# Kernel optimization log

Measured on AMD Instinct MI355X. Metric: run time of the kernel, lower is better.

Reference implementation:

```python
import jax, jax.numpy as jnp
import numpy as np

# Cayley-Dickson octonion multiplication tables (from the source module)
SIGN_TABLE = np.array([
    [+1, -1, -1, -1, -1, -1, -1, -1],
    [+1, +1, +1, -1, +1, -1, -1, +1],
    [+1, -1, +1, +1, +1, +1, -1, -1],
    [+1, +1, -1, +1, +1, -1, +1, -1],
    [+1, -1, -1, -1, +1, +1, +1, +1],
    [+1, +1, -1, +1, -1, +1, -1, +1],
    [+1, +1, +1, -1, -1, +1, +1, -1],
    [+1, -1, +1, +1, -1, -1, +1, +1],
], dtype=np.float32)
WEIGHT_IDX = np.array([
    [0, 1, 2, 3, 4, 5, 6, 7],
    [1, 0, 3, 2, 5, 4, 7, 6],
    [2, 3, 0, 1, 6, 7, 4, 5],
    [3, 2, 1, 0, 7, 6, 5, 4],
    [4, 5, 6, 7, 0, 1, 2, 3],
    [5, 4, 7, 6, 1, 0, 3, 2],
    [6, 7, 4, 5, 2, 3, 0, 1],
    [7, 6, 5, 4, 3, 2, 1, 0],
], dtype=np.int32)

B, T, D_IN, D_OUT = 4, 2048, 4096, 4096
K = D_IN // 8   # per-component input dim
N = D_OUT // 8  # per-component output dim


def setup_inputs() -> dict:
    key = jax.random.key(0)
    k1, k2 = jax.random.split(key)
    x = jax.random.normal(k1, (B, T, D_IN), dtype=jnp.float32)
    weight = jax.random.normal(k2, (8, N, K), dtype=jnp.float32) * (1.0 / np.sqrt(K))
    return {"x": x, "weight": weight}


def reference(x, weight):
    """Fused octonion (Cayley-Dickson) linear layer.

    y_i = sum_j sign[i,j] * x_j @ W[widx[i,j]].T
    x components are contiguous chunks of the last dim: x_j = x[..., j*K:(j+1)*K].
    """
    b, t, f = x.shape
    k = f // 8
    xs = x.reshape(b, t, 8, k)                 # [B,T,8,K], component axis j
    Wg = weight[jnp.asarray(WEIGHT_IDX)]        # [8(i),8(j),N,K] gathered weights
    S = jnp.asarray(SIGN_TABLE, dtype=x.dtype)  # [8(i),8(j)]
    # contract over j (component) and k (features); produce [B,T,i,N]
    y = jnp.einsum('ij,btjk,ijnk->btin', S, xs, Wg)
    return y.reshape(b, t, -1)                  # [B,T,8*N]
```

## Files before the change

### kernel.cpp

```cpp
#include <hip/hip_runtime.h>
#include <stdint.h>

typedef __attribute__((ext_vector_type(8))) short bf16x8;
typedef __attribute__((ext_vector_type(4))) float f32x4;

#define D_IN  4096
#define D_OUT 4096
#define KC 512
#define NC 512
#define NT 64

__constant__ float c_sign[64] = {
 +1,-1,-1,-1,-1,-1,-1,-1,
 +1,+1,+1,-1,+1,-1,-1,+1,
 +1,-1,+1,+1,+1,+1,-1,-1,
 +1,+1,-1,+1,+1,-1,+1,-1,
 +1,-1,-1,-1,+1,+1,+1,+1,
 +1,+1,-1,+1,-1,+1,-1,+1,
 +1,+1,+1,-1,-1,+1,+1,-1,
 +1,-1,+1,+1,-1,-1,+1,+1,
};

__device__ inline unsigned int pack2bf16(float a, float b) {
    unsigned int ua = __builtin_bit_cast(unsigned int, a);
    unsigned int ub = __builtin_bit_cast(unsigned int, b);
    ua = (ua + 0x7FFFu + ((ua >> 16) & 1u)) >> 16;
    ub = (ub + 0x7FFFu + ((ub >> 16) & 1u)) >> 16;
    return ua | (ub << 16);
}

typedef __attribute__((address_space(1))) const unsigned int gas_u32;
typedef __attribute__((address_space(3))) unsigned int las_u32;
#define ASYNC16(g, l) __builtin_amdgcn_global_load_lds((gas_u32*)(g), (las_u32*)(l), 16, 0, 0)
#define ENDP do { __builtin_amdgcn_s_barrier(); asm volatile("" ::: "memory"); } while (0)


__global__ __launch_bounds__(256)
void conv_x(const float* __restrict__ in, unsigned short* __restrict__ out, int n8) {
    int i = blockIdx.x * blockDim.x + threadIdx.x;
    if (i >= n8) return;
    const float4 a = ((const float4*)in)[(size_t)i * 2];
    const float4 b = ((const float4*)in)[(size_t)i * 2 + 1];
    uint4 o;
    o.x = pack2bf16(a.x, a.y); o.y = pack2bf16(a.z, a.w);
    o.z = pack2bf16(b.x, b.y); o.w = pack2bf16(b.z, b.w);
    ((uint4*)out)[i] = o;
}

__global__ __launch_bounds__(256)
void conv_w(const float* __restrict__ W, unsigned short* __restrict__ out) {
    int gid = blockIdx.x * blockDim.x + threadIdx.x;
    int row = gid >> 9;
    int c8  = gid & 511;
    int i = row >> 9, n = row & 511;
    int j = c8 >> 6;
    int k = (c8 & 63) << 3;
    float sgn = c_sign[i * 8 + j];
    const float* src = W + ((((i ^ j) * NC + n) * KC) + k);
    float4 a = *(const float4*)(src);
    float4 b = *(const float4*)(src + 4);
    uint4 o;
    o.x = pack2bf16(a.x * sgn, a.y * sgn); o.y = pack2bf16(a.z * sgn, a.w * sgn);
    o.z = pack2bf16(b.x * sgn, b.y * sgn); o.w = pack2bf16(b.z * sgn, b.w * sgn);
    ((uint4*)out)[gid] = o;
}


__device__ __forceinline__ void read_a(bf16x8 (&d)[4], const unsigned short* buf,
                                       int mh, int kk, int lane, int wr) {
#pragma unroll
    for (int f = 0; f < 4; ++f) {
        const int r  = wr * 128 + (mh * 4 + f) * 16 + (lane & 15);
        const int ch = (kk * 4 + (lane >> 4)) ^ (r & 7);
        d[f] = *(const bf16x8*)((const char*)buf + r * 128 + (ch << 4));
    }
}

__device__ __forceinline__ void read_b(bf16x8 (&d)[4], const unsigned short* buf,
                                       int kk, int lane, int wc) {
#pragma unroll
    for (int n = 0; n < 4; ++n) {
        const int r  = wc * 64 + n * 16 + (lane & 15);
        const int ch = (kk * 4 + (lane >> 4)) ^ (r & 7);
        d[n] = *(const bf16x8*)((const char*)buf + r * 128 + (ch << 4));
    }
}

__device__ __forceinline__ void mfma16(f32x4 (&acc)[8][4], int mh,
                                       const bf16x8 (&a)[4], const bf16x8 (&b)[4]) {
#pragma unroll
    for (int f = 0; f < 4; ++f)
#pragma unroll
        for (int n = 0; n < 4; ++n)
            acc[mh * 4 + f][n] = __builtin_amdgcn_mfma_f32_16x16x32_bf16(
                a[f], b[n], acc[mh * 4 + f][n], 0, 0, 0);
}

__device__ __forceinline__ void ktile_pipe(
    const unsigned short* Ac, const unsigned short* Bc,
    const unsigned short* An, const unsigned short* Bn,
    unsigned short* stA, unsigned short* stB,
    const unsigned short* gA1, const unsigned short* gB2,
    f32x4 (&acc)[8][4],
    bf16x8 (&aX)[4], bf16x8 (&aY)[4], bf16x8 (&bX)[4], bf16x8 (&bY)[4],
    size_t goff0, size_t goff1, int loff0, int loff1,
    int lane, int wr, int wc)
{
    read_a(aY, Ac, 1, 0, lane, wr);
    __builtin_amdgcn_s_setprio(1);
    mfma16(acc, 0, aX, bX);
    __builtin_amdgcn_s_setprio(0);
    read_a(aX, Ac, 0, 1, lane, wr);
    read_b(bY, Bc, 1, lane, wc);
    ASYNC16(gA1 + goff0, stA + loff0);
    ASYNC16(gA1 + goff1, stA + loff1);
    ASYNC16(gA1 + 128 * D_IN + goff0, stA + 8192 + loff0);
    ASYNC16(gA1 + 128 * D_IN + goff1, stA + 8192 + loff1);
    __builtin_amdgcn_s_setprio(1);
    mfma16(acc, 1, aY, bX);
    __builtin_amdgcn_s_setprio(0);
    ENDP;
    read_a(aY, Ac, 1, 1, lane, wr);
    ASYNC16(gB2 + goff0, stB + loff0);
    ASYNC16(gB2 + goff1, stB + loff1);
    __builtin_amdgcn_s_setprio(1);
    mfma16(acc, 0, aX, bY);
    __builtin_amdgcn_s_setprio(0);
    asm volatile("s_waitcnt vmcnt(2)");
    ENDP;
    read_a(aX, An, 0, 0, lane, wr);
    read_b(bX, Bn, 0, lane, wc);
    ASYNC16(gB2 + 128 * D_IN + goff0, stB + 8192 + loff0);
    ASYNC16(gB2 + 128 * D_IN + goff1, stB + 8192 + loff1);
    __builtin_amdgcn_s_setprio(1);
    mfma16(acc, 1, aY, bY);
    __builtin_amdgcn_s_setprio(0);
    ENDP;
}

__global__ __launch_bounds__(512, 2)
void octo_gemm_8ph(const unsigned short* __restrict__ Xb,
                   const unsigned short* __restrict__ Wb,
                   float* __restrict__ Y, int M)
{
    __shared__ __align__(16) unsigned short sm[65536];
    unsigned short* A0 = sm;
    unsigned short* A1 = sm + 16384;
    unsigned short* B0 = sm + 32768;
    unsigned short* B1 = sm + 49152;

    const int tid  = threadIdx.x;
    const int lane = tid & 63;
    const int wave = tid >> 6;
    const int wr   = wave >> 2;
    const int wc   = wave & 3;

    const int nbn = D_OUT / 256;
    const int nwg = (M / 256) * nbn;
    int bid = blockIdx.x;
    int cpx = nwg >> 3;
    int wg  = (bid & 7) * cpx + (bid >> 3);
    const int bm = wg / nbn, bn = wg % nbn;
    const int row0 = bm * 256, col0 = bn * 256;

    const int srow  = tid >> 3;
    const int sch   = tid & 7;
    const size_t goff0 = (size_t)srow * D_IN + (size_t)((sch ^ (srow & 7)) * 8);
    const size_t goff1 = goff0 + (size_t)64 * D_IN;
    const int loff0 = tid * 8;
    const int loff1 = loff0 + 4096;

    const unsigned short* gX = Xb + (size_t)row0 * D_IN;
    const unsigned short* gW = Wb + (size_t)col0 * D_IN;

    f32x4 acc[8][4];
    #pragma unroll
    for (int m = 0; m < 8; ++m)
        #pragma unroll
        for (int n = 0; n < 4; ++n)
            acc[m][n] = (f32x4){0.f, 0.f, 0.f, 0.f};

    ASYNC16(gX + goff0, A0 + loff0);              ASYNC16(gX + goff1, A0 + loff1);
    ASYNC16(gX + 128 * D_IN + goff0, A0 + 8192 + loff0);
    ASYNC16(gX + 128 * D_IN + goff1, A0 + 8192 + loff1);
    ASYNC16(gW + goff0, B0 + loff0);              ASYNC16(gW + goff1, B0 + loff1);
    ASYNC16(gW + 128 * D_IN + goff0, B0 + 8192 + loff0);
    ASYNC16(gW + 128 * D_IN + goff1, B0 + 8192 + loff1);
    ASYNC16(gW + 64 + goff0, B1 + loff0);         ASYNC16(gW + 64 + goff1, B1 + loff1);
    ASYNC16(gW + 64 + 128 * D_IN + goff0, B1 + 8192 + loff0);
    ASYNC16(gW + 64 + 128 * D_IN + goff1, B1 + 8192 + loff1);
    asm volatile("s_waitcnt vmcnt(4)");
    ENDP;

    bf16x8 aX[4], aY[4], bX[4], bY[4];
    read_a(aX, A0, 0, 0, lane, wr);
    read_b(bX, B0, 0, lane, wc);

    for (int i = 0; i < NT / 2; ++i) {
        const int u = 2 * i;
        const unsigned short* gA1t = gX + ((u + 1) & (NT - 1)) * 64;
        const unsigned short* gA2t = gX + ((u + 2) & (NT - 1)) * 64;
        const unsigned short* gB2t = gW + ((u + 2) & (NT - 1)) * 64;
        const unsigned short* gB3t = gW + ((u + 3) & (NT - 1)) * 64;

        ktile_pipe(A0, B0, A1, B1, A1, B0, gA1t, gB2t,
                   acc, aX, aY, bX, bY,
                   goff0, goff1, loff0, loff1, lane, wr, wc);
        ktile_pipe(A1, B1, A0, B0, A0, B1, gA2t, gB3t,
                   acc, aX, aY, bX, bY,
                   goff0, goff1, loff0, loff1, lane, wr, wc);
    }

    const int rl = (lane >> 4) << 2;
    const int cl = lane & 15;
    #pragma unroll
    for (int m = 0; m < 8; ++m) {
        const int rg = row0 + wr * 128 + m * 16 + rl;
        #pragma unroll
        for (int n = 0; n < 4; ++n) {
            const int cg = col0 + wc * 64 + n * 16 + cl;
            #pragma unroll
            for (int q = 0; q < 4; ++q)
                Y[(size_t)(rg + q) * D_OUT + cg] = acc[m][n][q];
        }
    }
}


#define BM 128
#define BN 128
#define BK 64

__global__ __launch_bounds__(256)
void octo_gemm_f32(const float* __restrict__ X, const float* __restrict__ W,
                   float* __restrict__ Y, int M)
{
    __shared__ __align__(16) unsigned short As[BM * BK];
    __shared__ __align__(16) unsigned short Bs[BN * BK];

    const int tid  = threadIdx.x;
    const int lane = tid & 63;
    const int wave = tid >> 6;
    const int wr   = wave >> 1;
    const int wc   = wave & 1;

    const int nbn = D_OUT / BN;
    const int nwg = (M / BM) * nbn;
    int bid = blockIdx.x;
    int wg  = bid;
    if ((nwg & 7) == 0) {
        int cpx = nwg >> 3;
        wg = (bid & 7) * cpx + (bid >> 3);
    }
    const int bm = wg / nbn, bn = wg % nbn;
    const int row0  = bm * BM;
    const int col0  = bn * BN;
    const int icomp = col0 >> 9;
    const int noff  = col0 & (NC - 1);

    const int srow = tid >> 4;
    const int scol = (tid & 15) << 2;

    f32x4 acc[4][4];
    #pragma unroll
    for (int m = 0; m < 4; ++m)
        #pragma unroll
        for (int n = 0; n < 4; ++n)
            acc[m][n] = (f32x4){0.f, 0.f, 0.f, 0.f};

    char* AsB = (char*)As;
    char* BsB = (char*)Bs;
    const int byteC = scol << 1;

    for (int step = 0; step < NT; ++step) {
        const int k0 = step * BK;
        const int j  = k0 >> 9;
        const int kc = k0 & (KC - 1);
        const float sgn = c_sign[icomp * 8 + j];
        const int   w   = icomp ^ j;
        const float* Wp = W + (((size_t)w * NC + noff) * KC + kc);
        const float* Xp = X + ((size_t)row0 * D_IN + k0);

        __syncthreads();
        #pragma unroll
        for (int p = 0; p < 8; ++p) {
            const int r  = p * 16 + srow;
            const int sb = r * 128 + ((((byteC >> 4) ^ (r & 7)) << 4)) + (byteC & 8);
            const float4 va = *(const float4*)(&Xp[(size_t)r * D_IN + scol]);
            *(uint2*)(AsB + sb) = make_uint2(pack2bf16(va.x, va.y),
                                             pack2bf16(va.z, va.w));
            const float4 vb = *(const float4*)(&Wp[(size_t)r * KC + scol]);
            *(uint2*)(BsB + sb) = make_uint2(pack2bf16(vb.x * sgn, vb.y * sgn),
                                             pack2bf16(vb.z * sgn, vb.w * sgn));
        }
        __syncthreads();

        #pragma unroll
        for (int kk = 0; kk < 2; ++kk) {
            bf16x8 af[4], bf[4];
            #pragma unroll
            for (int m = 0; m < 4; ++m) {
                const int r = wr * 64 + m * 16 + (lane & 15);
                const int chunk = (kk * 4 + (lane >> 4)) ^ (r & 7);
                af[m] = *(const bf16x8*)(AsB + r * 128 + (chunk << 4));
            }
            #pragma unroll
            for (int n = 0; n < 4; ++n) {
                const int r = wc * 64 + n * 16 + (lane & 15);
                const int chunk = (kk * 4 + (lane >> 4)) ^ (r & 7);
                bf[n] = *(const bf16x8*)(BsB + r * 128 + (chunk << 4));
            }
            #pragma unroll
            for (int m = 0; m < 4; ++m)
                #pragma unroll
                for (int n = 0; n < 4; ++n)
                    acc[m][n] = __builtin_amdgcn_mfma_f32_16x16x32_bf16(
                        af[m], bf[n], acc[m][n], 0, 0, 0);
        }
    }

    const int rl = (lane >> 4) << 2;
    const int cl = lane & 15;
    #pragma unroll
    for (int m = 0; m < 4; ++m) {
        const int rg = row0 + wr * 64 + m * 16 + rl;
        #pragma unroll
        for (int n = 0; n < 4; ++n) {
            const int cg = col0 + wc * 64 + n * 16 + cl;
            #pragma unroll
            for (int q = 0; q < 4; ++q)
                Y[(size_t)(rg + q) * D_OUT + cg] = acc[m][n][q];
        }
    }
}

extern "C" void kernel_launch(void* const* d_in, const int* in_sizes, int n_in,
                              void* d_out, int out_size, void* d_ws, size_t ws_size,
                              hipStream_t stream) {
    const float* X = (const float*)d_in[0];
    const float* W = (const float*)d_in[1];
    float* Y = (float*)d_out;
    const int M = in_sizes[0] / D_IN;

    const size_t xb_bytes = (size_t)M * D_IN * sizeof(unsigned short);
    const size_t wb_bytes = (size_t)D_OUT * D_IN * sizeof(unsigned short);

    if (ws_size >= xb_bytes + wb_bytes && (M % 256) == 0) {
        unsigned short* Xb = (unsigned short*)d_ws;
        unsigned short* Wb = (unsigned short*)((char*)d_ws + xb_bytes);
        const int n8x = M * D_IN / 8;
        hipLaunchKernelGGL(conv_x, dim3(n8x / 256), dim3(256), 0, stream, X, Xb, n8x);
        hipLaunchKernelGGL(conv_w, dim3((D_OUT * D_IN / 8) / 256), dim3(256), 0, stream, W, Wb);
        const int nwg = (M / 256) * (D_OUT / 256);
        hipLaunchKernelGGL(octo_gemm_8ph, dim3(nwg), dim3(512), 0, stream, Xb, Wb, Y, M);
    } else {
        const int nwg = (M / BM) * (D_OUT / BN);
        hipLaunchKernelGGL(octo_gemm_f32, dim3(nwg), dim3(256), 0, stream, X, W, Y, M);
    }
}
```

Baseline: 255.1 us.

## Merge conversion kernels, use nontemporal loads/stores, and reorder async prefetch in GEMM pipe

The separate X and W bf16 conversion kernels are merged into one launch that branches on block index, removing one kernel launch and its tail. Conversion loads and the GEMM output stores become nontemporal to reduce cache pollution. In the pipelined k-tile loop, the first pair of async A prefetches is issued earlier and an extra barrier is added, changing the overlap between MFMA and global-to-LDS copies. The added barrier may cost some synchronisation time, and the earlier writes into the staging buffer depend on the existing buffer rotation staying safe.

```diff
diff --git a/kernel.cpp b/kernel.cpp
--- a/kernel.cpp
+++ b/kernel.cpp
@@ -3,6 +3,7 @@
 
 typedef __attribute__((ext_vector_type(8))) short bf16x8;
 typedef __attribute__((ext_vector_type(4))) float f32x4;
+typedef __attribute__((ext_vector_type(4))) unsigned int u32x4;
 
 #define D_IN  4096
 #define D_OUT 4096
@@ -34,35 +35,36 @@
 #define ASYNC16(g, l) __builtin_amdgcn_global_load_lds((gas_u32*)(g), (las_u32*)(l), 16, 0, 0)
 #define ENDP do { __builtin_amdgcn_s_barrier(); asm volatile("" ::: "memory"); } while (0)
 
-
 __global__ __launch_bounds__(256)
-void conv_x(const float* __restrict__ in, unsigned short* __restrict__ out, int n8) {
-    int i = blockIdx.x * blockDim.x + threadIdx.x;
-    if (i >= n8) return;
-    const float4 a = ((const float4*)in)[(size_t)i * 2];
-    const float4 b = ((const float4*)in)[(size_t)i * 2 + 1];
-    uint4 o;
-    o.x = pack2bf16(a.x, a.y); o.y = pack2bf16(a.z, a.w);
-    o.z = pack2bf16(b.x, b.y); o.w = pack2bf16(b.z, b.w);
-    ((uint4*)out)[i] = o;
-}
-
-__global__ __launch_bounds__(256)
-void conv_w(const float* __restrict__ W, unsigned short* __restrict__ out) {
-    int gid = blockIdx.x * blockDim.x + threadIdx.x;
-    int row = gid >> 9;
-    int c8  = gid & 511;
-    int i = row >> 9, n = row & 511;
-    int j = c8 >> 6;
-    int k = (c8 & 63) << 3;
-    float sgn = c_sign[i * 8 + j];
-    const float* src = W + ((((i ^ j) * NC + n) * KC) + k);
-    float4 a = *(const float4*)(src);
-    float4 b = *(const float4*)(src + 4);
-    uint4 o;
-    o.x = pack2bf16(a.x * sgn, a.y * sgn); o.y = pack2bf16(a.z * sgn, a.w * sgn);
-    o.z = pack2bf16(b.x * sgn, b.y * sgn); o.w = pack2bf16(b.z * sgn, b.w * sgn);
-    ((uint4*)out)[gid] = o;
+void conv_xw(const float* __restrict__ X, const float* __restrict__ W,
+             unsigned short* __restrict__ Xb, unsigned short* __restrict__ Wb,
+             int nbx)
+{
+    if ((int)blockIdx.x < nbx) {
+        int i = blockIdx.x * 256 + threadIdx.x;
+        const f32x4* src = (const f32x4*)X + (size_t)i * 2;
+        const f32x4 a = __builtin_nontemporal_load(src);
+        const f32x4 b = __builtin_nontemporal_load(src + 1);
+        u32x4 o;
+        o.x = pack2bf16(a.x, a.y); o.y = pack2bf16(a.z, a.w);
+        o.z = pack2bf16(b.x, b.y); o.w = pack2bf16(b.z, b.w);
+        ((u32x4*)Xb)[i] = o;
+    } else {
+        int gid = (blockIdx.x - nbx) * 256 + threadIdx.x;
+        int row = gid >> 9;
+        int c8  = gid & 511;
+        int i = row >> 9, n = row & 511;
+        int j = c8 >> 6;
+        int k = (c8 & 63) << 3;
+        float sgn = c_sign[i * 8 + j];
+        const f32x4* src = (const f32x4*)(W + ((((i ^ j) * NC + n) * KC) + k));
+        const f32x4 a = __builtin_nontemporal_load(src);
+        const f32x4 b = __builtin_nontemporal_load(src + 1);
+        u32x4 o;
+        o.x = pack2bf16(a.x * sgn, a.y * sgn); o.y = pack2bf16(a.z * sgn, a.w * sgn);
+        o.z = pack2bf16(b.x * sgn, b.y * sgn); o.w = pack2bf16(b.z * sgn, b.w * sgn);
+        ((u32x4*)Wb)[gid] = o;
+    }
 }
 
 
@@ -107,13 +109,14 @@
     int lane, int wr, int wc)
 {
     read_a(aY, Ac, 1, 0, lane, wr);
+    ASYNC16(gA1 + goff0, stA + loff0);
+    ASYNC16(gA1 + goff1, stA + loff1);
     __builtin_amdgcn_s_setprio(1);
     mfma16(acc, 0, aX, bX);
     __builtin_amdgcn_s_setprio(0);
+    ENDP;
     read_a(aX, Ac, 0, 1, lane, wr);
     read_b(bY, Bc, 1, lane, wc);
-    ASYNC16(gA1 + goff0, stA + loff0);
-    ASYNC16(gA1 + goff1, stA + loff1);
     ASYNC16(gA1 + 128 * D_IN + goff0, stA + 8192 + loff0);
     ASYNC16(gA1 + 128 * D_IN + goff1, stA + 8192 + loff1);
     __builtin_amdgcn_s_setprio(1);
@@ -221,7 +224,8 @@
             const int cg = col0 + wc * 64 + n * 16 + cl;
             #pragma unroll
             for (int q = 0; q < 4; ++q)
-                Y[(size_t)(rg + q) * D_OUT + cg] = acc[m][n][q];
+                __builtin_nontemporal_store(acc[m][n][q],
+                                            &Y[(size_t)(rg + q) * D_OUT + cg]);
         }
     }
 }
@@ -348,9 +352,10 @@
     if (ws_size >= xb_bytes + wb_bytes && (M % 256) == 0) {
         unsigned short* Xb = (unsigned short*)d_ws;
         unsigned short* Wb = (unsigned short*)((char*)d_ws + xb_bytes);
-        const int n8x = M * D_IN / 8;
-        hipLaunchKernelGGL(conv_x, dim3(n8x / 256), dim3(256), 0, stream, X, Xb, n8x);
-        hipLaunchKernelGGL(conv_w, dim3((D_OUT * D_IN / 8) / 256), dim3(256), 0, stream, W, Wb);
+        const int nbx = (M * D_IN / 8) / 256;
+        const int nbw = ((D_OUT * D_IN / 8)) / 256;
+        hipLaunchKernelGGL(conv_xw, dim3(nbx + nbw), dim3(256), 0, stream,
+                           X, W, Xb, Wb, nbx);
         const int nwg = (M / 256) * (D_OUT / 256);
         hipLaunchKernelGGL(octo_gemm_8ph, dim3(nwg), dim3(512), 0, stream, Xb, Wb, Y, M);
     } else {
```

Result: slower. 265.1 us (+3.9%).
